# Optimization experiments

Measured on AMD Instinct MI355X. Metric: run time of the kernel, lower is better.

The kernel has to match this reference:

```python
import jax, jax.numpy as jnp
import numpy as np

B, TQ, TK, D, DV = 16, 2048, 2048, 128, 128
MASK_VAL = -1000000.0

def setup_inputs() -> dict:
    key = jax.random.key(0)
    kq, kk, kv, kl = jax.random.split(key, 4)
    q = jax.random.normal(kq, (B, TQ, D), dtype=jnp.float32)
    k = jax.random.normal(kk, (B, TK, D), dtype=jnp.float32)
    v = jax.random.normal(kv, (B, TK, DV), dtype=jnp.float32)
    valid_lens = jax.random.randint(kl, (B,), 1, TK, dtype=jnp.int64)
    return {"q": q, "k": k, "v": v, "valid_lens": valid_lens}

def reference(q, k, v, valid_lens):
    d = q.shape[-1]
    # scores: [B, Tq, Tk]
    scores = jnp.einsum('bqd,bkd->bqk', q, k) / jnp.sqrt(jnp.asarray(d, q.dtype))
    # mask key positions >= valid_len (same per-batch length for every query row)
    mask = jnp.arange(scores.shape[-1])[None, None, :] < valid_lens[:, None, None]
    scores = jnp.where(mask, scores, jnp.asarray(MASK_VAL, scores.dtype))
    attn = jax.nn.softmax(scores, axis=-1)
    # dropout p=0.0 (eval mode) -> identity
    return jnp.einsum('bqk,bkv->bqv', attn, v)
```

## Files before the change

kernel.cpp:

```cpp
#include <hip/hip_runtime.h>
#include <math.h>

#define NB 16
#define TQ 2048
#define TK 2048
#define DD 128
#define DVV 128

constexpr int KTILE = 32;
constexpr int QTILE = 128;

typedef __attribute__((ext_vector_type(8))) _Float16 half8;
typedef __attribute__((ext_vector_type(16))) float f32x16;
typedef __attribute__((ext_vector_type(4))) float f32x4;

__device__ inline float fast_exp2(float x) { return __builtin_amdgcn_exp2f(x); }
__device__ inline void setprio1() { __builtin_amdgcn_s_setprio(1); }
__device__ inline void setprio0() { __builtin_amdgcn_s_setprio(0); }

__device__ inline unsigned pk2(float a, float b) {
    auto h = __builtin_amdgcn_cvt_pkrtz(a, b);
    unsigned u;
    __builtin_memcpy(&u, &h, 4);
    return u;
}

__device__ inline void glds16(const _Float16* g, _Float16* l) {
    __builtin_amdgcn_global_load_lds(
        (const __attribute__((address_space(1))) void*)g,
        (__attribute__((address_space(3))) void*)l, 16, 0, 0);
}

__global__ __launch_bounds__(256)
void repack(const float* __restrict__ kg, const float* __restrict__ vg,
            const int* __restrict__ vlg,
            _Float16* __restrict__ Kpk, _Float16* __restrict__ Vpk)
{
    const int bt = blockIdx.x;
    const int b = bt >> 6, t = bt & 63;
    if (t * KTILE >= vlg[b]) return;
    const int tid = threadIdx.x;

    __shared__ float Vlds[32][129];

    const float* kin = kg + ((size_t)b * TK + t * KTILE) * DD;
    _Float16* kout = Kpk + ((size_t)bt << 12);
#pragma unroll
    for (int pp = 0; pp < 2; ++pp) {
        int s = tid + pp * 256;
        int c = s >> 6, l = s & 63;
        int row = l & 31, d0 = c * 16 + (l >> 5) * 8;
        const float* ip = kin + row * DD + d0;
        float4 f0 = *(const float4*)ip;
        float4 f1 = *(const float4*)(ip + 4);
        half8 hh;
        hh[0] = (_Float16)f0.x; hh[1] = (_Float16)f0.y;
        hh[2] = (_Float16)f0.z; hh[3] = (_Float16)f0.w;
        hh[4] = (_Float16)f1.x; hh[5] = (_Float16)f1.y;
        hh[6] = (_Float16)f1.z; hh[7] = (_Float16)f1.w;
        *(half8*)(kout + (size_t)s * 8) = hh;
    }

    const float* vin = vg + ((size_t)b * TK + t * KTILE) * DVV;
#pragma unroll
    for (int pp = 0; pp < 4; ++pp) {
        int idx = tid + pp * 256;
        int r = idx >> 5, c4 = (idx & 31) * 4;
        float4 f = *(const float4*)(vin + r * DVV + c4);
        Vlds[r][c4 + 0] = f.x; Vlds[r][c4 + 1] = f.y;
        Vlds[r][c4 + 2] = f.z; Vlds[r][c4 + 3] = f.w;
    }
    __syncthreads();
    _Float16* vout = Vpk + ((size_t)bt << 12);
#pragma unroll
    for (int pp = 0; pp < 2; ++pp) {
        int s = tid + pp * 256;
        int sv = s >> 6, l = s & 63;
        int dv = (sv >> 1) * 32 + (l & 31);
        int k0 = (sv & 1) * 16 + (l >> 5) * 8;
        half8 hh;
#pragma unroll
        for (int j = 0; j < 8; ++j)
            hh[j] = (_Float16)Vlds[k0 + j][dv];
        *(half8*)(vout + (size_t)s * 8) = hh;
    }
}

__global__ __launch_bounds__(256, 3)
void attn_fwd(const float* __restrict__ qg,
              const _Float16* __restrict__ Kpk, const _Float16* __restrict__ Vpk,
              const int* __restrict__ vlg,
              float* __restrict__ outg, _Float16* __restrict__ wso,
              float* __restrict__ wsml, int nsplit, int tpb)
{
    __shared__ __align__(16) _Float16 smem[24576];

    const int tid  = threadIdx.x;
    const int wid  = tid >> 6;
    const int lane = tid & 63;
    const int l31  = lane & 31;
    const int hi   = lane >> 5;

    const int b     = blockIdx.x & (NB - 1);
    const int qbase = (blockIdx.x >> 4) * QTILE;
    const int sp    = blockIdx.y;

    const int VL  = vlg[b];
    const int nkt = (VL + KTILE - 1) / KTILE;
    const int t0  = sp * tpb;
    const int t1  = min(nkt, t0 + tpb);
    if (t0 >= t1) return;

    const _Float16* ktb = Kpk + ((size_t)(b * 64) << 12);
    const _Float16* vtb = Vpk + ((size_t)(b * 64) << 12);

    half8 qf[8];
    {
        const float scale = 0.08838834764831845f * 1.4426950408889634f;
        const float* qp = qg + (size_t)(b * TQ + qbase + wid * 32 + l31) * DD;
#pragma unroll
        for (int c = 0; c < 8; ++c) {
            int d0 = c * 16 + hi * 8;
            float4 f0 = *(const float4*)(qp + d0);
            float4 f1 = *(const float4*)(qp + d0 + 4);
            half8 tq;
            tq[0] = (_Float16)(f0.x * scale); tq[1] = (_Float16)(f0.y * scale);
            tq[2] = (_Float16)(f0.z * scale); tq[3] = (_Float16)(f0.w * scale);
            tq[4] = (_Float16)(f1.x * scale); tq[5] = (_Float16)(f1.y * scale);
            tq[6] = (_Float16)(f1.z * scale); tq[7] = (_Float16)(f1.w * scale);
            qf[c] = tq;
        }
    }

    auto STAGE = [&](int buf, int t) {
        const _Float16* ks = ktb + ((size_t)t << 12) + wid * 1024 + lane * 8;
        const _Float16* vs = vtb + ((size_t)t << 12) + wid * 1024 + lane * 8;
        _Float16* kd = smem + buf * 4096 + wid * 1024;
        _Float16* vd = smem + 12288 + buf * 4096 + wid * 1024;
        glds16(ks, kd);
        glds16(ks + 512, kd + 512);
        glds16(vs, vd);
        glds16(vs + 512, vd + 512);
    };

    float m_i = -INFINITY, l_i = 0.f;
    f32x16 o[4];
#pragma unroll
    for (int n = 0; n < 4; ++n)
#pragma unroll
        for (int r = 0; r < 16; ++r) o[n][r] = 0.f;

    STAGE(0, t0);
    if (t0 + 1 < t1) STAGE(1, t0 + 1);

    int cur = 0;
    for (int t = t0; t < t1; ++t) {
        const bool h1 = (t + 1 < t1);
        const bool h2 = (t + 2 < t1);

        if (h1) asm volatile("s_waitcnt vmcnt(4)\ns_barrier" ::: "memory");
        else    asm volatile("s_waitcnt vmcnt(0)\ns_barrier" ::: "memory");

        if (h2) STAGE(cur == 0 ? 2 : cur - 1, t + 2);

        const _Float16* kbuf = smem + cur * 4096;
        const _Float16* vbuf = smem + 12288 + cur * 4096;
        const int kb = t * KTILE;

        f32x16 sc;
#pragma unroll
        for (int r = 0; r < 16; ++r) sc[r] = 0.f;
        setprio1();
#pragma unroll
        for (int c = 0; c < 8; ++c) {
            half8 kf = *(const half8*)(kbuf + c * 512 + lane * 8);
            sc = __builtin_amdgcn_mfma_f32_32x32x16_f16(kf, qf[c], sc, 0, 0, 0);
        }
        setprio0();

        if (kb + KTILE > VL) {
#pragma unroll
            for (int r = 0; r < 16; ++r) {
                int rowk = kb + (r & 3) + 8 * (r >> 2) + 4 * hi;
                if (rowk >= VL) sc[r] = -1e30f;
            }
        }

        float m8[8];
#pragma unroll
        for (int r = 0; r < 8; ++r) m8[r] = fmaxf(sc[r], sc[r + 8]);
        float m4[4];
#pragma unroll
        for (int r = 0; r < 4; ++r) m4[r] = fmaxf(m8[r], m8[r + 4]);
        float mx = fmaxf(fmaxf(m4[0], m4[1]), fmaxf(m4[2], m4[3]));
        mx = fmaxf(mx, __shfl_xor(mx, 32));

        const bool skip = __all(mx <= m_i + 8.0f);
        const float mnew = skip ? m_i : fmaxf(m_i, mx);

        float p[16];
#pragma unroll
        for (int r = 0; r < 16; ++r)
            p[r] = fast_exp2(sc[r] - mnew);
        float s8[8];
#pragma unroll
        for (int r = 0; r < 8; ++r) s8[r] = p[r] + p[r + 8];
        float s4[4];
#pragma unroll
        for (int r = 0; r < 4; ++r) s4[r] = s8[r] + s8[r + 4];
        float sum = (s4[0] + s4[1]) + (s4[2] + s4[3]);
        sum += __shfl_xor(sum, 32);

        unsigned a0 = pk2(p[0],  p[1]),  a1 = pk2(p[2],  p[3]);
        unsigned a2 = pk2(p[4],  p[5]),  a3 = pk2(p[6],  p[7]);
        unsigned b0 = pk2(p[8],  p[9]),  b1 = pk2(p[10], p[11]);
        unsigned b2 = pk2(p[12], p[13]), b3 = pk2(p[14], p[15]);
        unsigned pa0 = __shfl_xor(a0, 32), pa1 = __shfl_xor(a1, 32);
        unsigned pa2 = __shfl_xor(a2, 32), pa3 = __shfl_xor(a3, 32);
        unsigned pb0 = __shfl_xor(b0, 32), pb1 = __shfl_xor(b1, 32);
        unsigned pb2 = __shfl_xor(b2, 32), pb3 = __shfl_xor(b3, 32);
        union PF { unsigned u[4]; half8 v; } pf0, pf1;
        pf0.u[0] = hi ? pa2 : a0;  pf0.u[1] = hi ? pa3 : a1;
        pf0.u[2] = hi ? a2  : pa0; pf0.u[3] = hi ? a3  : pa1;
        pf1.u[0] = hi ? pb2 : b0;  pf1.u[1] = hi ? pb3 : b1;
        pf1.u[2] = hi ? b2  : pb0; pf1.u[3] = hi ? b3  : pb1;

        if (skip) {
            l_i += sum;
        } else {
            const float corr = fast_exp2(m_i - mnew);
            l_i = l_i * corr + sum;
            m_i = mnew;
#pragma unroll
            for (int n = 0; n < 4; ++n)
#pragma unroll
                for (int r = 0; r < 16; ++r) o[n][r] *= corr;
        }

        setprio1();
#pragma unroll
        for (int n = 0; n < 4; ++n) {
            half8 v0 = *(const half8*)(vbuf + (n * 2 + 0) * 512 + lane * 8);
            o[n] = __builtin_amdgcn_mfma_f32_32x32x16_f16(v0, pf0.v, o[n], 0, 0, 0);
            half8 v1 = *(const half8*)(vbuf + (n * 2 + 1) * 512 + lane * 8);
            o[n] = __builtin_amdgcn_mfma_f32_32x32x16_f16(v1, pf1.v, o[n], 0, 0, 0);
        }
        setprio0();

        cur = (cur == 2) ? 0 : cur + 1;
    }

    if (nsplit == 1) {
        const float inv = 1.0f / l_i;
        float* op = outg + (size_t)(b * TQ + qbase + wid * 32 + l31) * DVV;
#pragma unroll
        for (int n = 0; n < 4; ++n)
#pragma unroll
            for (int g = 0; g < 4; ++g) {
                int d0 = n * 32 + g * 8 + hi * 4;
                f32x4 vv = {o[n][g * 4 + 0] * inv, o[n][g * 4 + 1] * inv,
                            o[n][g * 4 + 2] * inv, o[n][g * 4 + 3] * inv};
                *(f32x4*)(op + d0) = vv;
            }
    } else {
        _Float16* po = wso + ((size_t)(sp * NB + b) * TQ + qbase + wid * 32 + l31) * DVV;
#pragma unroll
        for (int n = 0; n < 4; ++n)
#pragma unroll
            for (int g = 0; g < 4; ++g) {
                int d0 = n * 32 + g * 8 + hi * 4;
                union { unsigned u[2]; double d; } hv;
                hv.u[0] = pk2(o[n][g * 4 + 0], o[n][g * 4 + 1]);
                hv.u[1] = pk2(o[n][g * 4 + 2], o[n][g * 4 + 3]);
                *(double*)(po + d0) = hv.d;
            }
        if (hi == 0) {
            int q = qbase + wid * 32 + l31;
            *(float2*)&wsml[((size_t)(sp * NB + b) * TQ + q) * 2] = make_float2(m_i, l_i);
        }
    }
}

__global__ __launch_bounds__(256)
void attn_combine(const _Float16* __restrict__ wso, const float* __restrict__ wsml,
                  const int* __restrict__ vlg, float* __restrict__ outg, int tpb)
{
    const int idx = blockIdx.x * 256 + threadIdx.x;
    const int d8 = idx & 15;
    const int q  = (idx >> 4) & (TQ - 1);
    const int b  = idx >> 15;

    const int VL  = vlg[b];
    const int nkt = (VL + KTILE - 1) / KTILE;
    const int nv  = (nkt + tpb - 1) / tpb;

    float M = -1e30f, den = 0.f;
    float acc[8] = {0.f, 0.f, 0.f, 0.f, 0.f, 0.f, 0.f, 0.f};
    for (int s = 0; s < nv; ++s) {
        const size_t row = (size_t)(s * NB + b) * TQ + q;
        float2 ml = *(const float2*)&wsml[row * 2];
        float Mn = fmaxf(M, ml.x);
        float c  = fast_exp2(M - Mn);
        float w  = fast_exp2(ml.x - Mn);
        half8 ov = *(const half8*)&wso[row * DVV + d8 * 8];
#pragma unroll
        for (int j = 0; j < 8; ++j)
            acc[j] = acc[j] * c + (float)ov[j] * w;
        den = den * c + w * ml.y;
        M = Mn;
    }
    const float inv = 1.0f / den;
    float* op = outg + ((size_t)b * TQ + q) * DVV + d8 * 8;
    f32x4 r0 = {acc[0] * inv, acc[1] * inv, acc[2] * inv, acc[3] * inv};
    f32x4 r1 = {acc[4] * inv, acc[5] * inv, acc[6] * inv, acc[7] * inv};
    *(f32x4*)op = r0;
    *(f32x4*)(op + 4) = r1;
}

extern "C" void kernel_launch(void* const* d_in, const int* in_sizes, int n_in,
                              void* d_out, int out_size, void* d_ws, size_t ws_size,
                              hipStream_t stream) {
    const float* q  = (const float*)d_in[0];
    const float* k  = (const float*)d_in[1];
    const float* v  = (const float*)d_in[2];
    const int*   vl = (const int*)d_in[3];
    float* out = (float*)d_out;

    const size_t pk_elems  = (size_t)NB * 64 * 4096;
    const size_t pk_bytes  = 2 * pk_elems * sizeof(_Float16);
    const size_t o_elems   = (size_t)NB * TQ * DVV;
    const size_t per_split = o_elems * sizeof(_Float16)
                           + (size_t)NB * TQ * 2 * sizeof(float);

    int ns = 1;
    if      (ws_size >= pk_bytes + 8 * per_split) ns = 8;
    else if (ws_size >= pk_bytes + 4 * per_split) ns = 4;
    else if (ws_size >= pk_bytes + 2 * per_split) ns = 2;
    const int tpb = 64 / ns;

    _Float16* Kpk = (_Float16*)d_ws;
    _Float16* Vpk = Kpk + pk_elems;
    _Float16* wso = Vpk + pk_elems;
    float*   wsml = (float*)(wso + (size_t)ns * o_elems);

    hipLaunchKernelGGL(repack, dim3(NB * 64), dim3(256), 0, stream,
                       k, v, vl, Kpk, Vpk);

    dim3 grid(NB * (TQ / QTILE), ns);
    hipLaunchKernelGGL(attn_fwd, grid, dim3(256), 0, stream,
                       q, Kpk, Vpk, vl, out, wso, wsml, ns, tpb);

    if (ns > 1) {
        dim3 cgrid((NB * TQ * 16) / 256);
        hipLaunchKernelGGL(attn_combine, cgrid, dim3(256), 0, stream,
                           wso, wsml, vl, out, tpb);
    }
}
```

Baseline: 78.11 us.

## Software-pipeline QK^T one tile ahead of softmax and PV

```diff
diff --git a/kernel.cpp b/kernel.cpp
--- a/kernel.cpp
+++ b/kernel.cpp
@@ -86,7 +86,7 @@
     }
 }
 
-__global__ __launch_bounds__(256, 3)
+__global__ __launch_bounds__(256, 2)
 void attn_fwd(const float* __restrict__ qg,
               const _Float16* __restrict__ Kpk, const _Float16* __restrict__ Vpk,
               const int* __restrict__ vlg,
@@ -142,6 +142,16 @@
         glds16(vs, vd);
         glds16(vs + 512, vd + 512);
     };
+    auto QKT = [&](f32x16& sc, int buf) {
+        const _Float16* kbuf = smem + buf * 4096;
+        setprio1();
+#pragma unroll
+        for (int c = 0; c < 8; ++c) {
+            half8 kf = *(const half8*)(kbuf + c * 512 + lane * 8);
+            sc = __builtin_amdgcn_mfma_f32_32x32x16_f16(kf, qf[c], sc, 0, 0, 0);
+        }
+        setprio0();
+    };
 
     float m_i = -INFINITY, l_i = 0.f;
     f32x16 o[4];
@@ -151,44 +161,45 @@
         for (int r = 0; r < 16; ++r) o[n][r] = 0.f;
 
     STAGE(0, t0);
-    if (t0 + 1 < t1) STAGE(1, t0 + 1);
+    if (t0 + 1 < t1) {
+        STAGE(1, t0 + 1);
+        asm volatile("s_waitcnt vmcnt(4)\ns_barrier" ::: "memory");
+    } else {
+        asm volatile("s_waitcnt vmcnt(0)\ns_barrier" ::: "memory");
+    }
+
+    f32x16 scA, scB;
+#pragma unroll
+    for (int r = 0; r < 16; ++r) scA[r] = 0.f;
+    QKT(scA, 0);
 
     int cur = 0;
     for (int t = t0; t < t1; ++t) {
         const bool h1 = (t + 1 < t1);
         const bool h2 = (t + 2 < t1);
-
-        if (h1) asm volatile("s_waitcnt vmcnt(4)\ns_barrier" ::: "memory");
-        else    asm volatile("s_waitcnt vmcnt(0)\ns_barrier" ::: "memory");
-
-        if (h2) STAGE(cur == 0 ? 2 : cur - 1, t + 2);
-
-        const _Float16* kbuf = smem + cur * 4096;
-        const _Float16* vbuf = smem + 12288 + cur * 4096;
+        int nxt = (cur == 2) ? 0 : cur + 1;
+        int nn2 = (nxt == 2) ? 0 : nxt + 1;
+
+        if (h1) {
+            asm volatile("s_waitcnt vmcnt(0)\ns_barrier" ::: "memory");
+            if (h2) STAGE(nn2, t + 2);
+#pragma unroll
+            for (int r = 0; r < 16; ++r) scB[r] = 0.f;
+            QKT(scB, nxt);
+        }
+
         const int kb = t * KTILE;
-
-        f32x16 sc;
-#pragma unroll
-        for (int r = 0; r < 16; ++r) sc[r] = 0.f;
-        setprio1();
-#pragma unroll
-        for (int c = 0; c < 8; ++c) {
-            half8 kf = *(const half8*)(kbuf + c * 512 + lane * 8);
-            sc = __builtin_amdgcn_mfma_f32_32x32x16_f16(kf, qf[c], sc, 0, 0, 0);
-        }
-        setprio0();
-
         if (kb + KTILE > VL) {
 #pragma unroll
             for (int r = 0; r < 16; ++r) {
                 int rowk = kb + (r & 3) + 8 * (r >> 2) + 4 * hi;
-                if (rowk >= VL) sc[r] = -1e30f;
+                if (rowk >= VL) scA[r] = -1e30f;
             }
         }
 
         float m8[8];
 #pragma unroll
-        for (int r = 0; r < 8; ++r) m8[r] = fmaxf(sc[r], sc[r + 8]);
+        for (int r = 0; r < 8; ++r) m8[r] = fmaxf(scA[r], scA[r + 8]);
         float m4[4];
 #pragma unroll
         for (int r = 0; r < 4; ++r) m4[r] = fmaxf(m8[r], m8[r + 4]);
@@ -201,7 +212,7 @@
         float p[16];
 #pragma unroll
         for (int r = 0; r < 16; ++r)
-            p[r] = fast_exp2(sc[r] - mnew);
+            p[r] = fast_exp2(scA[r] - mnew);
         float s8[8];
 #pragma unroll
         for (int r = 0; r < 8; ++r) s8[r] = p[r] + p[r + 8];
@@ -237,6 +248,7 @@
                 for (int r = 0; r < 16; ++r) o[n][r] *= corr;
         }
 
+        const _Float16* vbuf = smem + 12288 + cur * 4096;
         setprio1();
 #pragma unroll
         for (int n = 0; n < 4; ++n) {
@@ -247,7 +259,8 @@
         }
         setprio0();
 
-        cur = (cur == 2) ? 0 : cur + 1;
+        if (h1) scA = scB;
+        cur = nxt;
     }
 
     if (nsplit == 1) {
```

Measured after the change: 78.64 us. Within noise of the previous version (+0.7%).

## Double the key tile per attention iteration and switch to double-buffered staging

Applied to the files above, without the earlier changes.

```diff
diff --git a/kernel.cpp b/kernel.cpp
--- a/kernel.cpp
+++ b/kernel.cpp
@@ -7,7 +7,7 @@
 #define DD 128
 #define DVV 128
 
-constexpr int KTILE = 32;
+constexpr int KTILE = 64;
 constexpr int QTILE = 128;
 
 typedef __attribute__((ext_vector_type(8))) _Float16 half8;
@@ -38,12 +38,12 @@
 {
     const int bt = blockIdx.x;
     const int b = bt >> 6, t = bt & 63;
-    if (t * KTILE >= vlg[b]) return;
+    if (t * 32 >= vlg[b]) return;
     const int tid = threadIdx.x;
 
     __shared__ float Vlds[32][129];
 
-    const float* kin = kg + ((size_t)b * TK + t * KTILE) * DD;
+    const float* kin = kg + ((size_t)b * TK + t * 32) * DD;
     _Float16* kout = Kpk + ((size_t)bt << 12);
 #pragma unroll
     for (int pp = 0; pp < 2; ++pp) {
@@ -61,7 +61,7 @@
         *(half8*)(kout + (size_t)s * 8) = hh;
     }
 
-    const float* vin = vg + ((size_t)b * TK + t * KTILE) * DVV;
+    const float* vin = vg + ((size_t)b * TK + t * 32) * DVV;
 #pragma unroll
     for (int pp = 0; pp < 4; ++pp) {
         int idx = tid + pp * 256;
@@ -86,14 +86,14 @@
     }
 }
 
-__global__ __launch_bounds__(256, 3)
+__global__ __launch_bounds__(256, 2)
 void attn_fwd(const float* __restrict__ qg,
               const _Float16* __restrict__ Kpk, const _Float16* __restrict__ Vpk,
               const int* __restrict__ vlg,
               float* __restrict__ outg, _Float16* __restrict__ wso,
               float* __restrict__ wsml, int nsplit, int tpb)
 {
-    __shared__ __align__(16) _Float16 smem[24576];
+    __shared__ __align__(16) _Float16 smem[32768];
 
     const int tid  = threadIdx.x;
     const int wid  = tid >> 6;
@@ -133,14 +133,15 @@
     }
 
     auto STAGE = [&](int buf, int t) {
-        const _Float16* ks = ktb + ((size_t)t << 12) + wid * 1024 + lane * 8;
-        const _Float16* vs = vtb + ((size_t)t << 12) + wid * 1024 + lane * 8;
-        _Float16* kd = smem + buf * 4096 + wid * 1024;
-        _Float16* vd = smem + 12288 + buf * 4096 + wid * 1024;
-        glds16(ks, kd);
-        glds16(ks + 512, kd + 512);
-        glds16(vs, vd);
-        glds16(vs + 512, vd + 512);
+        const _Float16* ks = ktb + ((size_t)(2 * t) << 12) + wid * 2048 + lane * 8;
+        const _Float16* vs = vtb + ((size_t)(2 * t) << 12) + wid * 2048 + lane * 8;
+        _Float16* kd = smem + buf * 8192 + wid * 2048;
+        _Float16* vd = smem + 16384 + buf * 8192 + wid * 2048;
+#pragma unroll
+        for (int u = 0; u < 4; ++u) {
+            glds16(ks + u * 512, kd + u * 512);
+            glds16(vs + u * 512, vd + u * 512);
+        }
     };
 
     float m_i = -INFINITY, l_i = 0.f;
@@ -151,30 +152,28 @@
         for (int r = 0; r < 16; ++r) o[n][r] = 0.f;
 
     STAGE(0, t0);
-    if (t0 + 1 < t1) STAGE(1, t0 + 1);
-
     int cur = 0;
     for (int t = t0; t < t1; ++t) {
         const bool h1 = (t + 1 < t1);
-        const bool h2 = (t + 2 < t1);
-
-        if (h1) asm volatile("s_waitcnt vmcnt(4)\ns_barrier" ::: "memory");
+        if (h1) STAGE(cur ^ 1, t + 1);
+
+        if (h1) asm volatile("s_waitcnt vmcnt(8)\ns_barrier" ::: "memory");
         else    asm volatile("s_waitcnt vmcnt(0)\ns_barrier" ::: "memory");
 
-        if (h2) STAGE(cur == 0 ? 2 : cur - 1, t + 2);
-
-        const _Float16* kbuf = smem + cur * 4096;
-        const _Float16* vbuf = smem + 12288 + cur * 4096;
+        const _Float16* kbuf = smem + cur * 8192;
+        const _Float16* vbuf = smem + 16384 + cur * 8192;
         const int kb = t * KTILE;
 
-        f32x16 sc;
-#pragma unroll
-        for (int r = 0; r < 16; ++r) sc[r] = 0.f;
+        f32x16 scA, scB;
+#pragma unroll
+        for (int r = 0; r < 16; ++r) { scA[r] = 0.f; scB[r] = 0.f; }
         setprio1();
 #pragma unroll
         for (int c = 0; c < 8; ++c) {
-            half8 kf = *(const half8*)(kbuf + c * 512 + lane * 8);
-            sc = __builtin_amdgcn_mfma_f32_32x32x16_f16(kf, qf[c], sc, 0, 0, 0);
+            half8 kfA = *(const half8*)(kbuf + c * 512 + lane * 8);
+            scA = __builtin_amdgcn_mfma_f32_32x32x16_f16(kfA, qf[c], scA, 0, 0, 0);
+            half8 kfB = *(const half8*)(kbuf + 4096 + c * 512 + lane * 8);
+            scB = __builtin_amdgcn_mfma_f32_32x32x16_f16(kfB, qf[c], scB, 0, 0, 0);
         }
         setprio0();
 
@@ -182,13 +181,17 @@
 #pragma unroll
             for (int r = 0; r < 16; ++r) {
                 int rowk = kb + (r & 3) + 8 * (r >> 2) + 4 * hi;
-                if (rowk >= VL) sc[r] = -1e30f;
+                if (rowk >= VL) scA[r] = -1e30f;
+                if (rowk + 32 >= VL) scB[r] = -1e30f;
             }
         }
 
+        float m16[16];
+#pragma unroll
+        for (int r = 0; r < 16; ++r) m16[r] = fmaxf(scA[r], scB[r]);
         float m8[8];
 #pragma unroll
-        for (int r = 0; r < 8; ++r) m8[r] = fmaxf(sc[r], sc[r + 8]);
+        for (int r = 0; r < 8; ++r) m8[r] = fmaxf(m16[r], m16[r + 8]);
         float m4[4];
 #pragma unroll
         for (int r = 0; r < 4; ++r) m4[r] = fmaxf(m8[r], m8[r + 4]);
@@ -198,32 +201,53 @@
         const bool skip = __all(mx <= m_i + 8.0f);
         const float mnew = skip ? m_i : fmaxf(m_i, mx);
 
-        float p[16];
-#pragma unroll
-        for (int r = 0; r < 16; ++r)
-            p[r] = fast_exp2(sc[r] - mnew);
+        float pA[16], pB[16];
+#pragma unroll
+        for (int r = 0; r < 16; ++r) {
+            pA[r] = fast_exp2(scA[r] - mnew);
+            pB[r] = fast_exp2(scB[r] - mnew);
+        }
+        float s16[16];
+#pragma unroll
+        for (int r = 0; r < 16; ++r) s16[r] = pA[r] + pB[r];
         float s8[8];
 #pragma unroll
-        for (int r = 0; r < 8; ++r) s8[r] = p[r] + p[r + 8];
+        for (int r = 0; r < 8; ++r) s8[r] = s16[r] + s16[r + 8];
         float s4[4];
 #pragma unroll
         for (int r = 0; r < 4; ++r) s4[r] = s8[r] + s8[r + 4];
         float sum = (s4[0] + s4[1]) + (s4[2] + s4[3]);
         sum += __shfl_xor(sum, 32);
 
-        unsigned a0 = pk2(p[0],  p[1]),  a1 = pk2(p[2],  p[3]);
-        unsigned a2 = pk2(p[4],  p[5]),  a3 = pk2(p[6],  p[7]);
-        unsigned b0 = pk2(p[8],  p[9]),  b1 = pk2(p[10], p[11]);
-        unsigned b2 = pk2(p[12], p[13]), b3 = pk2(p[14], p[15]);
-        unsigned pa0 = __shfl_xor(a0, 32), pa1 = __shfl_xor(a1, 32);
-        unsigned pa2 = __shfl_xor(a2, 32), pa3 = __shfl_xor(a3, 32);
-        unsigned pb0 = __shfl_xor(b0, 32), pb1 = __shfl_xor(b1, 32);
-        unsigned pb2 = __shfl_xor(b2, 32), pb3 = __shfl_xor(b3, 32);
-        union PF { unsigned u[4]; half8 v; } pf0, pf1;
-        pf0.u[0] = hi ? pa2 : a0;  pf0.u[1] = hi ? pa3 : a1;
-        pf0.u[2] = hi ? a2  : pa0; pf0.u[3] = hi ? a3  : pa1;
-        pf1.u[0] = hi ? pb2 : b0;  pf1.u[1] = hi ? pb3 : b1;
-        pf1.u[2] = hi ? b2  : pb0; pf1.u[3] = hi ? b3  : pb1;
+        union PF { unsigned u[4]; half8 v; } pfA0, pfA1, pfB0, pfB1;
+        {
+            unsigned a0 = pk2(pA[0],  pA[1]),  a1 = pk2(pA[2],  pA[3]);
+            unsigned a2 = pk2(pA[4],  pA[5]),  a3 = pk2(pA[6],  pA[7]);
+            unsigned b0 = pk2(pA[8],  pA[9]),  b1 = pk2(pA[10], pA[11]);
+            unsigned b2 = pk2(pA[12], pA[13]), b3 = pk2(pA[14], pA[15]);
+            unsigned xa0 = __shfl_xor(a0, 32), xa1 = __shfl_xor(a1, 32);
+            unsigned xa2 = __shfl_xor(a2, 32), xa3 = __shfl_xor(a3, 32);
+            unsigned xb0 = __shfl_xor(b0, 32), xb1 = __shfl_xor(b1, 32);
+            unsigned xb2 = __shfl_xor(b2, 32), xb3 = __shfl_xor(b3, 32);
+            pfA0.u[0] = hi ? xa2 : a0;  pfA0.u[1] = hi ? xa3 : a1;
+            pfA0.u[2] = hi ? a2  : xa0; pfA0.u[3] = hi ? a3  : xa1;
+            pfA1.u[0] = hi ? xb2 : b0;  pfA1.u[1] = hi ? xb3 : b1;
+            pfA1.u[2] = hi ? b2  : xb0; pfA1.u[3] = hi ? b3  : xb1;
+        }
+        {
+            unsigned a0 = pk2(pB[0],  pB[1]),  a1 = pk2(pB[2],  pB[3]);
+            unsigned a2 = pk2(pB[4],  pB[5]),  a3 = pk2(pB[6],  pB[7]);
+            unsigned b0 = pk2(pB[8],  pB[9]),  b1 = pk2(pB[10], pB[11]);
+            unsigned b2 = pk2(pB[12], pB[13]), b3 = pk2(pB[14], pB[15]);
+            unsigned xa0 = __shfl_xor(a0, 32), xa1 = __shfl_xor(a1, 32);
+            unsigned xa2 = __shfl_xor(a2, 32), xa3 = __shfl_xor(a3, 32);
+            unsigned xb0 = __shfl_xor(b0, 32), xb1 = __shfl_xor(b1, 32);
+            unsigned xb2 = __shfl_xor(b2, 32), xb3 = __shfl_xor(b3, 32);
+            pfB0.u[0] = hi ? xa2 : a0;  pfB0.u[1] = hi ? xa3 : a1;
+            pfB0.u[2] = hi ? a2  : xa0; pfB0.u[3] = hi ? a3  : xa1;
+            pfB1.u[0] = hi ? xb2 : b0;  pfB1.u[1] = hi ? xb3 : b1;
+            pfB1.u[2] = hi ? b2  : xb0; pfB1.u[3] = hi ? b3  : xb1;
+        }
 
         if (skip) {
             l_i += sum;
@@ -241,13 +265,18 @@
 #pragma unroll
         for (int n = 0; n < 4; ++n) {
             half8 v0 = *(const half8*)(vbuf + (n * 2 + 0) * 512 + lane * 8);
-            o[n] = __builtin_amdgcn_mfma_f32_32x32x16_f16(v0, pf0.v, o[n], 0, 0, 0);
+            o[n] = __builtin_amdgcn_mfma_f32_32x32x16_f16(v0, pfA0.v, o[n], 0, 0, 0);
             half8 v1 = *(const half8*)(vbuf + (n * 2 + 1) * 512 + lane * 8);
-            o[n] = __builtin_amdgcn_mfma_f32_32x32x16_f16(v1, pf1.v, o[n], 0, 0, 0);
+            o[n] = __builtin_amdgcn_mfma_f32_32x32x16_f16(v1, pfA1.v, o[n], 0, 0, 0);
+            half8 v2 = *(const half8*)(vbuf + 4096 + (n * 2 + 0) * 512 + lane * 8);
+            o[n] = __builtin_amdgcn_mfma_f32_32x32x16_f16(v2, pfB0.v, o[n], 0, 0, 0);
+            half8 v3 = *(const half8*)(vbuf + 4096 + (n * 2 + 1) * 512 + lane * 8);
+            o[n] = __builtin_amdgcn_mfma_f32_32x32x16_f16(v3, pfB1.v, o[n], 0, 0, 0);
         }
         setprio0();
 
-        cur = (cur == 2) ? 0 : cur + 1;
+        asm volatile("s_waitcnt lgkmcnt(0)\ns_barrier" ::: "memory");
+        cur ^= 1;
     }
 
     if (nsplit == 1) {
@@ -336,7 +365,7 @@
     if      (ws_size >= pk_bytes + 8 * per_split) ns = 8;
     else if (ws_size >= pk_bytes + 4 * per_split) ns = 4;
     else if (ws_size >= pk_bytes + 2 * per_split) ns = 2;
-    const int tpb = 64 / ns;
+    const int tpb = 32 / ns;
 
     _Float16* Kpk = (_Float16*)d_ws;
     _Float16* Vpk = Kpk + pk_elems;
```

New measurement: 83.07 us. 1.06x slower.
